# Optimization experiments

Hardware: AMD Instinct MI355X
Metric: run time of the kernel (lower is better)

## Reference

```python
import jax, jax.numpy as jnp
import numpy as np

TOP_K = 3
TEMP = 5.0
EPS = 1e-12

def _normalize(x):
    # F.normalize(dim=-1): x / max(||x||_2, eps)
    n = jnp.linalg.norm(x, axis=-1, keepdims=True)
    return x / jnp.maximum(n, EPS)

def setup_inputs() -> dict:
    key = jax.random.key(0)
    ks = jax.random.split(key, 6)
    B, D, P = 32768, 512, 4096
    return {
        "regime_vector": jax.random.normal(ks[0], (B, D), dtype=jnp.float32),
        "prototypes": jax.random.normal(ks[1], (P, D), dtype=jnp.float32) * 0.1,
        "W1": jax.random.normal(ks[2], (32, 2 * D), dtype=jnp.float32) * 0.02,
        "b1": jax.random.normal(ks[3], (32,), dtype=jnp.float32) * 0.01,
        "W2": jax.random.normal(ks[4], (16, 32), dtype=jnp.float32) * 0.1,
        "b2": jax.random.normal(ks[5], (16,), dtype=jnp.float32) * 0.01,
    }

def reference(regime_vector, prototypes, W1, b1, W2, b2):
    # Cosine similarities: [B, P]
    sims = _normalize(regime_vector) @ _normalize(prototypes).T
    top_sims, top_idx = jax.lax.top_k(sims, TOP_K)          # [B, K]
    weights = jax.nn.softmax(top_sims * TEMP, axis=-1)       # [B, K]
    # Gather candidate prototypes: [B, K, D]
    cand = prototypes[top_idx]
    # Concat(regime, pattern) along feature dim: [B, K, 2D]
    B, K, D = cand.shape
    combined = jnp.concatenate(
        [jnp.broadcast_to(regime_vector[:, None, :], (B, K, D)), cand], axis=-1)
    # Two-layer MLP (torch Linear: x @ W.T + b)
    h = jax.nn.relu(jnp.einsum('bkd,hd->bkh', combined, W1) + b1)  # [B, K, 32]
    feats = jnp.einsum('bkh,oh->bko', h, W2) + b2                  # [B, K, 16]
    # Softmax-weighted sum over the K candidates
    pattern_features = jnp.einsum('bk,bko->bo', weights, feats)    # [B, 16]
    return pattern_features
```

## Files before the change

### kernel.cpp

```cpp
#include <hip/hip_runtime.h>
#include <stdint.h>


#define BDIM 512
#define NB   32768
#define NP   4096

typedef float  f32x4 __attribute__((ext_vector_type(4)));
typedef short  s16x8 __attribute__((ext_vector_type(8)));
typedef unsigned short u16;

__device__ __forceinline__ u16 f2bf(float f) {
  uint32_t u = __float_as_uint(f);
  return (u16)((u + 0x7FFFu + ((u >> 16) & 1u)) >> 16);
}
__device__ __forceinline__ uint32_t mapbf(uint32_t h) {
  return h ^ ((h & 0x8000u) ? 0xFFFFu : 0x8000u);
}
__device__ __forceinline__ uint32_t umx(uint32_t a, uint32_t b) { return a > b ? a : b; }
__device__ __forceinline__ uint32_t umn(uint32_t a, uint32_t b) { return a > b ? b : a; }

__device__ __forceinline__ void ins8(uint32_t* t, uint32_t k) {
#pragma unroll
  for (int i = 0; i < 8; ++i) {
    uint32_t mx = umx(t[i], k), mn = umn(t[i], k);
    t[i] = mx; k = mn;
  }
}

__device__ __forceinline__ void bmerge(uint32_t* a, const uint32_t* b) {
  uint32_t t[8];
#pragma unroll
  for (int i = 0; i < 8; ++i) t[i] = umx(a[i], b[7 - i]);
#pragma unroll
  for (int i = 0; i < 4; ++i) { uint32_t x = umx(t[i], t[i + 4]), y = umn(t[i], t[i + 4]); t[i] = x; t[i + 4] = y; }
#pragma unroll
  for (int g = 0; g < 8; g += 4)
#pragma unroll
    for (int i = 0; i < 2; ++i) { uint32_t x = umx(t[g + i], t[g + i + 2]), y = umn(t[g + i], t[g + i + 2]); t[g + i] = x; t[g + i + 2] = y; }
#pragma unroll
  for (int p = 0; p < 8; p += 2) { uint32_t x = umx(t[p], t[p + 1]), y = umn(t[p], t[p + 1]); t[p] = x; t[p + 1] = y; }
#pragma unroll
  for (int i = 0; i < 8; ++i) a[i] = t[i];
}

__device__ __forceinline__ void mergeshfl(uint32_t* a, int mask) {
  uint32_t b[8];
#pragma unroll
  for (int i = 0; i < 8; ++i) b[i] = (uint32_t)__shfl_xor((int)a[i], mask, 64);
  bmerge(a, b);
}

__global__ __launch_bounds__(256) void prep_kernel(
    const float* __restrict__ src, const float* __restrict__ W1, int w1_off,
    u16* __restrict__ obf, float* __restrict__ onrm, float* __restrict__ oproj,
    float* __restrict__ onf32 )
{
  __shared__ float rows[16][512];
  __shared__ float scratch[8][32];
  const int t = threadIdx.x, l = t & 63, w = t >> 6;
  const long rowbase = (long)blockIdx.x * 16;

  {
    const int r = t >> 4, c0 = (t & 15) * 32;
    const float4* gp = (const float4*)(src + (rowbase + r) * BDIM + c0);
    float4* dp = (float4*)&rows[r][c0];
#pragma unroll
    for (int i = 0; i < 8; ++i) dp[i] = gp[i];
  }
  float wreg[64];
  {
    const int h = t & 31, seg = t >> 5;
    const float* wp = W1 + h * 1024 + w1_off + seg * 64;
#pragma unroll
    for (int i = 0; i < 64; ++i) wreg[i] = wp[i];
  }
  __syncthreads();

#pragma unroll
  for (int i = 0; i < 4; ++i) {
    const int r = w * 4 + i;
    float4 a = *(const float4*)&rows[r][4 * l];
    float4 c = *(const float4*)&rows[r][256 + 4 * l];
    float ss = a.x * a.x + a.y * a.y + a.z * a.z + a.w * a.w
             + c.x * c.x + c.y * c.y + c.z * c.z + c.w * c.w;
#pragma unroll
    for (int msk = 1; msk < 64; msk <<= 1) ss += __shfl_xor(ss, msk, 64);
    const float n = fmaxf(sqrtf(ss), 1e-12f);
    if (l == 0) onrm[rowbase + r] = n;
    float4 qa, qc;
    qa.x = a.x / n; qa.y = a.y / n; qa.z = a.z / n; qa.w = a.w / n;
    qc.x = c.x / n; qc.y = c.y / n; qc.z = c.z / n; qc.w = c.w / n;
    ushort4 u0, u1;
    u0.x = f2bf(qa.x); u0.y = f2bf(qa.y); u0.z = f2bf(qa.z); u0.w = f2bf(qa.w);
    u1.x = f2bf(qc.x); u1.y = f2bf(qc.y); u1.z = f2bf(qc.z); u1.w = f2bf(qc.w);
    *(ushort4*)(obf + (rowbase + r) * BDIM + 4 * l) = u0;
    *(ushort4*)(obf + (rowbase + r) * BDIM + 256 + 4 * l) = u1;
    if (onf32) {
      *(float4*)(onf32 + (rowbase + r) * BDIM + 4 * l) = qa;
      *(float4*)(onf32 + (rowbase + r) * BDIM + 256 + 4 * l) = qc;
    }
  }

  const int h = t & 31, seg = t >> 5;
  for (int r = 0; r < 16; ++r) {
    float p = 0.f;
#pragma unroll
    for (int i = 0; i < 16; ++i) {
      const float4 rv = *(const float4*)&rows[r][seg * 64 + 4 * i];
      p = fmaf(wreg[4 * i + 0], rv.x, p);
      p = fmaf(wreg[4 * i + 1], rv.y, p);
      p = fmaf(wreg[4 * i + 2], rv.z, p);
      p = fmaf(wreg[4 * i + 3], rv.w, p);
    }
    scratch[seg][h] = p;
    __syncthreads();
    if (t < 32) {
      float s2 = 0.f;
#pragma unroll
      for (int sg = 0; sg < 8; ++sg) s2 += scratch[sg][t];
      oproj[(rowbase + r) * 32 + t] = s2;
    }
    __syncthreads();
  }
}

__global__ __launch_bounds__(512, 2) void topk_kernel(
    const u16* __restrict__ An,
    const u16* __restrict__ Bn,
    int* __restrict__ top8out)
{
  __shared__ uint4 smem[3648];
  uint4* As = smem;
  uint4* Bs = smem + 512;
  u16*   dmp = (u16*)(smem + 2560);
  uint32_t* mb = (uint32_t*)smem;

  const int t = threadIdx.x;
  const int l = t & 63;
  const int wid = t >> 6;
  const int wm = wid >> 2;
  const int wn = wid & 3;
  const int g = l >> 4;
  const int m = l & 15;
  const long rb = (long)blockIdx.x * 128;

  const int ar = t >> 2, ac = t & 3;
  const uint4* Agp = (const uint4*)An + (rb + ar) * 64 + ac;
  const uint4* Bgp = (const uint4*)Bn;

  int aIdx[4], bIdx[8];
#pragma unroll
  for (int fm = 0; fm < 4; ++fm) aIdx[fm] = g * 128 + wm * 64 + fm * 16 + m;
#pragma unroll
  for (int fn = 0; fn < 8; ++fn) bIdx[fn] = g * 512 + wn * 128 + fn * 16 + m;

  uint32_t t8[4][8];
#pragma unroll
  for (int a = 0; a < 4; ++a)
#pragma unroll
    for (int i = 0; i < 8; ++i) t8[a][i] = 0u;

  uint4 pa = Agp[0];
  uint4 pb0 = Bgp[(0 + ar) * 64 + ac];
  uint4 pb1 = Bgp[(128 + ar) * 64 + ac];
  uint4 pb2 = Bgp[(256 + ar) * 64 + ac];
  uint4 pb3 = Bgp[(384 + ar) * 64 + ac];

  for (int ni = 0; ni < 8; ++ni) {
    const int n0 = ni * 512;
    f32x4 acc[4][8];
#pragma unroll
    for (int fm = 0; fm < 4; ++fm)
#pragma unroll
      for (int fn = 0; fn < 8; ++fn) acc[fm][fn] = (f32x4){0.f, 0.f, 0.f, 0.f};

    for (int kt = 0; kt < 16; ++kt) {
      __syncthreads();
      As[ac * 128 + ar] = pa;
      Bs[ac * 512 + ar] = pb0;
      Bs[ac * 512 + 128 + ar] = pb1;
      Bs[ac * 512 + 256 + ar] = pb2;
      Bs[ac * 512 + 384 + ar] = pb3;
      {
        int nkt = kt + 1, nni = ni;
        if (nkt == 16) { nkt = 0; ++nni; if (nni == 8) nni = 0; }
        pa = Agp[nkt * 4];
        const long bb = ((long)nni * 512 + ar) * 64 + nkt * 4 + ac;
        pb0 = Bgp[bb];
        pb1 = Bgp[bb + 128 * 64];
        pb2 = Bgp[bb + 256 * 64];
        pb3 = Bgp[bb + 384 * 64];
      }
      __syncthreads();
      uint4 a4[4];
#pragma unroll
      for (int fm = 0; fm < 4; ++fm) a4[fm] = As[aIdx[fm]];
#pragma unroll
      for (int h = 0; h < 2; ++h) {
        uint4 b4[4];
#pragma unroll
        for (int i = 0; i < 4; ++i) b4[i] = Bs[bIdx[4 * h + i]];
#pragma unroll
        for (int fm = 0; fm < 4; ++fm)
#pragma unroll
          for (int i = 0; i < 4; ++i)
            acc[fm][4 * h + i] = __builtin_amdgcn_mfma_f32_16x16x32_bf16(
                __builtin_bit_cast(s16x8, a4[fm]),
                __builtin_bit_cast(s16x8, b4[i]),
                acc[fm][4 * h + i], 0, 0, 0);
      }
    }

#pragma unroll
    for (int fm = 0; fm < 4; ++fm) {
#pragma unroll
      for (int h = 0; h < 2; ++h) {
#pragma unroll
        for (int fi = 0; fi < 4; ++fi)
#pragma unroll
          for (int r = 0; r < 4; ++r)
            dmp[(wid * 16 + 4 * g + r) * 68 + 16 * fi + m] = f2bf(acc[fm][4 * h + fi][r]);
        asm volatile("s_waitcnt lgkmcnt(0)" ::: "memory");
        const int colb = n0 + wn * 128 + h * 64 + g * 16;
#pragma unroll
        for (int j = 0; j < 4; ++j) {
          const uint2 v = *(const uint2*)(dmp + (wid * 16 + m) * 68 + g * 16 + 4 * j);
          const uint32_t k0 = (mapbf(v.x & 0xFFFFu) << 16) | (uint32_t)(colb + 4 * j + 0);
          const uint32_t k1 = (mapbf(v.x >> 16)     << 16) | (uint32_t)(colb + 4 * j + 1);
          const uint32_t k2 = (mapbf(v.y & 0xFFFFu) << 16) | (uint32_t)(colb + 4 * j + 2);
          const uint32_t k3 = (mapbf(v.y >> 16)     << 16) | (uint32_t)(colb + 4 * j + 3);
          const uint32_t mx = umx(umx(k0, k1), umx(k2, k3));
          if (mx > t8[fm][7]) {
            ins8(t8[fm], k0); ins8(t8[fm], k1); ins8(t8[fm], k2); ins8(t8[fm], k3);
          }
        }
      }
    }
  }

  __syncthreads();
#pragma unroll
  for (int fm = 0; fm < 4; ++fm) {
    uint32_t cur[8];
#pragma unroll
    for (int i = 0; i < 8; ++i) cur[i] = t8[fm][i];
    mergeshfl(cur, 16);
    mergeshfl(cur, 32);
    if (l < 16) {
      const int row = wm * 64 + fm * 16 + m;
      uint32_t* dst = mb + row * 36 + wn * 8;
      uint4 u0; u0.x = cur[0]; u0.y = cur[1]; u0.z = cur[2]; u0.w = cur[3];
      uint4 u1; u1.x = cur[4]; u1.y = cur[5]; u1.z = cur[6]; u1.w = cur[7];
      *(uint4*)(dst) = u0;
      *(uint4*)(dst + 4) = u1;
    }
  }
  __syncthreads();
  if (t < 128) {
    const int row = t;
    const uint32_t* src = mb + row * 36;
    uint32_t A8[8], B8[8], C8[8], D8[8];
#pragma unroll
    for (int i = 0; i < 8; ++i) { A8[i] = src[i]; B8[i] = src[8 + i]; C8[i] = src[16 + i]; D8[i] = src[24 + i]; }
    bmerge(A8, B8); bmerge(C8, D8); bmerge(A8, C8);
    int* outp = top8out + (rb + row) * 8;
#pragma unroll
    for (int i = 0; i < 8; ++i) outp[i] = (int)(A8[i] & 0xFFFu);
  }
}

__global__ __launch_bounds__(256) void finalize_kernel(
    const float* __restrict__ regime, const float* __restrict__ protoNf,
    const int* __restrict__ top8, const float* __restrict__ nrm_r,
    const float* __restrict__ rproj, const float* __restrict__ cproj,
    const float* __restrict__ b1, const float* __restrict__ W2,
    const float* __restrict__ b2, float* __restrict__ out)
{
  __shared__ float rlds[4][512];
  const int t = threadIdx.x, l = t & 63, w = t >> 6;
  const long b = (long)blockIdx.x * 4 + w;

  {
    const float n = nrm_r[b];
    const float4* gp = (const float4*)(regime + b * BDIM);
    float4 v0 = gp[l], v1 = gp[64 + l];
    v0.x /= n; v0.y /= n; v0.z /= n; v0.w /= n;
    v1.x /= n; v1.y /= n; v1.z /= n; v1.w /= n;
    *(float4*)&rlds[w][4 * l] = v0;
    *(float4*)&rlds[w][256 + 4 * l] = v1;
  }
  __syncthreads();

  const int j = l >> 3;
  const int pj = top8[b * 8 + j];
  double dd = 0.0;
  {
    const float4* pp = (const float4*)(protoNf + (long)pj * BDIM);
    const float4* rr = (const float4*)&rlds[w][0];
#pragma unroll
    for (int u = 0; u < 16; ++u) {
      const float4 p4 = pp[(l & 7) + 8 * u];
      const float4 r4 = rr[(l & 7) + 8 * u];
      dd = fma((double)p4.x, (double)r4.x, dd);
      dd = fma((double)p4.y, (double)r4.y, dd);
      dd = fma((double)p4.z, (double)r4.z, dd);
      dd = fma((double)p4.w, (double)r4.w, dd);
    }
  }
  dd += __shfl_xor(dd, 1, 64);
  dd += __shfl_xor(dd, 2, 64);
  dd += __shfl_xor(dd, 4, 64);

  double sall[8]; int pall[8];
#pragma unroll
  for (int q = 0; q < 8; ++q) {
    sall[q] = __shfl(dd, q * 8, 64);
    pall[q] = __shfl(pj, q * 8, 64);
  }
  double vv[3]; int ppi[3]; unsigned chosen = 0;
#pragma unroll
  for (int r = 0; r < 3; ++r) {
    double bv = -1e300; int bp = 0x7FFFFFFF; int bq = 0;
#pragma unroll
    for (int q = 0; q < 8; ++q) {
      const bool ex = (chosen >> q) & 1u;
      const bool better = !ex && ((sall[q] > bv) || (sall[q] == bv && pall[q] < bp));
      bv = better ? sall[q] : bv;
      bp = better ? pall[q] : bp;
      bq = better ? q : bq;
    }
    vv[r] = bv; ppi[r] = bp; chosen |= 1u << bq;
  }
  const float v0f = (float)vv[0], v1f = (float)vv[1], v2f = (float)vv[2];
  const float e1 = expf(5.f * (v1f - v0f));
  const float e2 = expf(5.f * (v2f - v0f));
  const float winv = 1.f / (1.f + e1 + e2);
  const float w0 = winv, w1 = e1 * winv, w2 = e2 * winv;

  const int hu = l & 31, o = l & 15;
  const float rpv = rproj[b * 32 + hu];
  const float b1v = b1[hu];
  float w2row[32];
#pragma unroll
  for (int hh = 0; hh < 32; ++hh) w2row[hh] = W2[o * 32 + hh];
  float outacc = (l < 16) ? b2[o] : 0.f;
#pragma unroll
  for (int k = 0; k < 3; ++k) {
    const float cpv = cproj[(long)ppi[k] * 32 + hu];
    const float hval = fmaxf(rpv + cpv + b1v, 0.f);
    float f = 0.f;
#pragma unroll
    for (int hh = 0; hh < 32; ++hh) f = fmaf(w2row[hh], __shfl(hval, hh, 64), f);
    const float wk = (k == 0) ? w0 : ((k == 1) ? w1 : w2);
    outacc = fmaf(wk, f, outacc);
  }
  if (l < 16) out[b * 16 + o] = outacc;
}

extern "C" void kernel_launch(void* const* d_in, const int* in_sizes, int n_in,
                              void* d_out, int out_size, void* d_ws, size_t ws_size,
                              hipStream_t stream)
{
  (void)in_sizes; (void)n_in; (void)out_size; (void)ws_size;
  const float* regime = (const float*)d_in[0];
  const float* protos = (const float*)d_in[1];
  const float* W1     = (const float*)d_in[2];
  const float* b1     = (const float*)d_in[3];
  const float* W2     = (const float*)d_in[4];
  const float* b2     = (const float*)d_in[5];
  float* out = (float*)d_out;

  char* ws = (char*)d_ws;
  u16*   protoN  = (u16*)ws;    ws += (size_t)NP * BDIM * 2;
  u16*   regimeN = (u16*)ws;    ws += (size_t)NB * BDIM * 2;
  float* nrm_p   = (float*)ws;  ws += (size_t)NP * 4;
  float* nrm_r   = (float*)ws;  ws += (size_t)NB * 4;
  float* cproj   = (float*)ws;  ws += (size_t)NP * 32 * 4;
  float* rproj   = (float*)ws;  ws += (size_t)NB * 32 * 4;
  int*   top8    = (int*)ws;    ws += (size_t)NB * 8 * 4;
  float* protoNf = (float*)ws;

  hipLaunchKernelGGL(prep_kernel, dim3(NP / 16), dim3(256), 0, stream,
                     protos, W1, 512, protoN, nrm_p, cproj, protoNf);
  hipLaunchKernelGGL(prep_kernel, dim3(NB / 16), dim3(256), 0, stream,
                     regime, W1, 0, regimeN, nrm_r, rproj, (float*)nullptr);
  hipLaunchKernelGGL(topk_kernel, dim3(NB / 128), dim3(512), 0, stream,
                     regimeN, protoN, top8);
  hipLaunchKernelGGL(finalize_kernel, dim3(NB / 4), dim3(256), 0, stream,
                     regime, protoNf, top8, nrm_r, rproj, cproj, b1, W2, b2, out);
}
```

Before: 480.4 us.

## Rewrite top-k GEMM with direct global-to-LDS double buffering and fp32 top-3 keys

```diff
diff --git a/kernel.cpp b/kernel.cpp
--- a/kernel.cpp
+++ b/kernel.cpp
@@ -5,27 +5,35 @@
 #define BDIM 512
 #define NB   32768
 #define NP   4096
+#define PCH  256
 
 typedef float  f32x4 __attribute__((ext_vector_type(4)));
 typedef short  s16x8 __attribute__((ext_vector_type(8)));
 typedef unsigned short u16;
 
+typedef const __attribute__((address_space(1))) unsigned int* gas_t;
+typedef __attribute__((address_space(3))) unsigned int* las_t;
+
+__device__ __forceinline__ void gll16(const void* g, void* l) {
+  __builtin_amdgcn_global_load_lds((gas_t)g, (las_t)l, 16, 0, 0);
+}
+
 __device__ __forceinline__ u16 f2bf(float f) {
   uint32_t u = __float_as_uint(f);
   return (u16)((u + 0x7FFFu + ((u >> 16) & 1u)) >> 16);
 }
-__device__ __forceinline__ uint32_t mapbf(uint32_t h) {
-  return h ^ ((h & 0x8000u) ? 0xFFFFu : 0x8000u);
-}
 __device__ __forceinline__ uint32_t umx(uint32_t a, uint32_t b) { return a > b ? a : b; }
 __device__ __forceinline__ uint32_t umn(uint32_t a, uint32_t b) { return a > b ? b : a; }
 
-__device__ __forceinline__ void ins8(uint32_t* t, uint32_t k) {
-#pragma unroll
-  for (int i = 0; i < 8; ++i) {
-    uint32_t mx = umx(t[i], k), mn = umn(t[i], k);
-    t[i] = mx; k = mn;
-  }
+__device__ __forceinline__ uint32_t packkey(float v, int col) {
+  uint32_t u = __float_as_uint(v);
+  uint32_t mp = u ^ (uint32_t)(((int)u >> 31) | 0x80000000);
+  return (mp & 0xFFFFF000u) | (uint32_t)col;
+}
+__device__ __forceinline__ float unpackf(uint32_t k) {
+  uint32_t mbits = k & 0xFFFFF000u;
+  uint32_t u = (mbits & 0x80000000u) ? (mbits ^ 0x80000000u) : ~mbits;
+  return __uint_as_float(u);
 }
 
 __device__ __forceinline__ void bmerge(uint32_t* a, const uint32_t* b) {
@@ -43,7 +51,6 @@
 #pragma unroll
   for (int i = 0; i < 8; ++i) a[i] = t[i];
 }
-
 __device__ __forceinline__ void mergeshfl(uint32_t* a, int mask) {
   uint32_t b[8];
 #pragma unroll
@@ -53,11 +60,11 @@
 
 __global__ __launch_bounds__(256) void prep_kernel(
     const float* __restrict__ src, const float* __restrict__ W1, int w1_off,
-    u16* __restrict__ obf, float* __restrict__ onrm, float* __restrict__ oproj,
-    float* __restrict__ onf32 )
+    int mode, u16* __restrict__ obf, float* __restrict__ onrm,
+    float* __restrict__ oproj, float* __restrict__ onf32)
 {
   __shared__ float rows[16][512];
-  __shared__ float scratch[8][32];
+  __shared__ float pscr[16][8][32];
   const int t = threadIdx.x, l = t & 63, w = t >> 6;
   const long rowbase = (long)blockIdx.x * 16;
 
@@ -80,6 +87,7 @@
 #pragma unroll
   for (int i = 0; i < 4; ++i) {
     const int r = w * 4 + i;
+    const long row = rowbase + r;
     float4 a = *(const float4*)&rows[r][4 * l];
     float4 c = *(const float4*)&rows[r][256 + 4 * l];
     float ss = a.x * a.x + a.y * a.y + a.z * a.z + a.w * a.w
@@ -87,18 +95,22 @@
 #pragma unroll
     for (int msk = 1; msk < 64; msk <<= 1) ss += __shfl_xor(ss, msk, 64);
     const float n = fmaxf(sqrtf(ss), 1e-12f);
-    if (l == 0) onrm[rowbase + r] = n;
     float4 qa, qc;
     qa.x = a.x / n; qa.y = a.y / n; qa.z = a.z / n; qa.w = a.w / n;
     qc.x = c.x / n; qc.y = c.y / n; qc.z = c.z / n; qc.w = c.w / n;
     ushort4 u0, u1;
     u0.x = f2bf(qa.x); u0.y = f2bf(qa.y); u0.z = f2bf(qa.z); u0.w = f2bf(qa.w);
     u1.x = f2bf(qc.x); u1.y = f2bf(qc.y); u1.z = f2bf(qc.z); u1.w = f2bf(qc.w);
-    *(ushort4*)(obf + (rowbase + r) * BDIM + 4 * l) = u0;
-    *(ushort4*)(obf + (rowbase + r) * BDIM + 256 + 4 * l) = u1;
-    if (onf32) {
-      *(float4*)(onf32 + (rowbase + r) * BDIM + 4 * l) = qa;
-      *(float4*)(onf32 + (rowbase + r) * BDIM + 256 + 4 * l) = qc;
+    if (mode == 0) {
+      if (l == 0) onrm[row] = n;
+      *(ushort4*)(obf + row * BDIM + 4 * l) = u0;
+      *(ushort4*)(obf + row * BDIM + 256 + 4 * l) = u1;
+    } else {
+      char* base = (char*)obf;
+      *(ushort4*)(base + ((long)(l >> 4) * NP + row) * 128 + 8 * (l & 15)) = u0;
+      *(ushort4*)(base + ((long)(4 + (l >> 4)) * NP + row) * 128 + 8 * (l & 15)) = u1;
+      *(float4*)(onf32 + row * BDIM + 4 * l) = qa;
+      *(float4*)(onf32 + row * BDIM + 256 + 4 * l) = qc;
     }
   }
 
@@ -106,173 +118,172 @@
   for (int r = 0; r < 16; ++r) {
     float p = 0.f;
 #pragma unroll
-    for (int i = 0; i < 16; ++i) {
-      const float4 rv = *(const float4*)&rows[r][seg * 64 + 4 * i];
-      p = fmaf(wreg[4 * i + 0], rv.x, p);
-      p = fmaf(wreg[4 * i + 1], rv.y, p);
-      p = fmaf(wreg[4 * i + 2], rv.z, p);
-      p = fmaf(wreg[4 * i + 3], rv.w, p);
-    }
-    scratch[seg][h] = p;
-    __syncthreads();
-    if (t < 32) {
-      float s2 = 0.f;
-#pragma unroll
-      for (int sg = 0; sg < 8; ++sg) s2 += scratch[sg][t];
-      oproj[(rowbase + r) * 32 + t] = s2;
-    }
-    __syncthreads();
-  }
-}
-
-__global__ __launch_bounds__(512, 2) void topk_kernel(
-    const u16* __restrict__ An,
-    const u16* __restrict__ Bn,
-    int* __restrict__ top8out)
+    for (int j = 0; j < 16; ++j) {
+      const float4 rv = *(const float4*)&rows[r][seg * 64 + 4 * j];
+      p = fmaf(wreg[4 * j + 0], rv.x, p);
+      p = fmaf(wreg[4 * j + 1], rv.y, p);
+      p = fmaf(wreg[4 * j + 2], rv.z, p);
+      p = fmaf(wreg[4 * j + 3], rv.w, p);
+    }
+    pscr[r][seg][h] = p;
+  }
+  __syncthreads();
+#pragma unroll
+  for (int q = 0; q < 2; ++q) {
+    const int idx = t + q * 256;
+    const int rr = idx >> 5, hh = idx & 31;
+    float s = 0.f;
+#pragma unroll
+    for (int sg = 0; sg < 8; ++sg) s += pscr[rr][sg][hh];
+    oproj[(rowbase + rr) * 32 + hh] = s;
+  }
+}
+
+__global__ __launch_bounds__(256, 2) void topk_kernel(
+    const u16* __restrict__ Rn,
+    const u16* __restrict__ Pk,
+    uint32_t* __restrict__ keys8)
 {
-  __shared__ uint4 smem[3648];
-  uint4* As = smem;
-  uint4* Bs = smem + 512;
-  u16*   dmp = (u16*)(smem + 2560);
-  uint32_t* mb = (uint32_t*)smem;
-
-  const int t = threadIdx.x;
-  const int l = t & 63;
-  const int wid = t >> 6;
-  const int wm = wid >> 2;
-  const int wn = wid & 3;
-  const int g = l >> 4;
-  const int m = l & 15;
-  const long rb = (long)blockIdx.x * 128;
-
-  const int ar = t >> 2, ac = t & 3;
-  const uint4* Agp = (const uint4*)An + (rb + ar) * 64 + ac;
-  const uint4* Bgp = (const uint4*)Bn;
-
-  int aIdx[4], bIdx[8];
-#pragma unroll
-  for (int fm = 0; fm < 4; ++fm) aIdx[fm] = g * 128 + wm * 64 + fm * 16 + m;
-#pragma unroll
-  for (int fn = 0; fn < 8; ++fn) bIdx[fn] = g * 512 + wn * 128 + fn * 16 + m;
-
-  uint32_t t8[4][8];
-#pragma unroll
-  for (int a = 0; a < 4; ++a)
-#pragma unroll
-    for (int i = 0; i < 8; ++i) t8[a][i] = 0u;
-
-  uint4 pa = Agp[0];
-  uint4 pb0 = Bgp[(0 + ar) * 64 + ac];
-  uint4 pb1 = Bgp[(128 + ar) * 64 + ac];
-  uint4 pb2 = Bgp[(256 + ar) * 64 + ac];
-  uint4 pb3 = Bgp[(384 + ar) * 64 + ac];
-
-  for (int ni = 0; ni < 8; ++ni) {
-    const int n0 = ni * 512;
-    f32x4 acc[4][8];
-#pragma unroll
-    for (int fm = 0; fm < 4; ++fm)
-#pragma unroll
-      for (int fn = 0; fn < 8; ++fn) acc[fm][fn] = (f32x4){0.f, 0.f, 0.f, 0.f};
-
-    for (int kt = 0; kt < 16; ++kt) {
-      __syncthreads();
-      As[ac * 128 + ar] = pa;
-      Bs[ac * 512 + ar] = pb0;
-      Bs[ac * 512 + 128 + ar] = pb1;
-      Bs[ac * 512 + 256 + ar] = pb2;
-      Bs[ac * 512 + 384 + ar] = pb3;
-      {
-        int nkt = kt + 1, nni = ni;
-        if (nkt == 16) { nkt = 0; ++nni; if (nni == 8) nni = 0; }
-        pa = Agp[nkt * 4];
-        const long bb = ((long)nni * 512 + ar) * 64 + nkt * 4 + ac;
-        pb0 = Bgp[bb];
-        pb1 = Bgp[bb + 128 * 64];
-        pb2 = Bgp[bb + 256 * 64];
-        pb3 = Bgp[bb + 384 * 64];
-      }
-      __syncthreads();
-      uint4 a4[4];
-#pragma unroll
-      for (int fm = 0; fm < 4; ++fm) a4[fm] = As[aIdx[fm]];
-#pragma unroll
-      for (int h = 0; h < 2; ++h) {
-        uint4 b4[4];
-#pragma unroll
-        for (int i = 0; i < 4; ++i) b4[i] = Bs[bIdx[4 * h + i]];
-#pragma unroll
-        for (int fm = 0; fm < 4; ++fm)
-#pragma unroll
-          for (int i = 0; i < 4; ++i)
-            acc[fm][4 * h + i] = __builtin_amdgcn_mfma_f32_16x16x32_bf16(
-                __builtin_bit_cast(s16x8, a4[fm]),
-                __builtin_bit_cast(s16x8, b4[i]),
-                acc[fm][4 * h + i], 0, 0, 0);
-      }
-    }
-
-#pragma unroll
-    for (int fm = 0; fm < 4; ++fm) {
-#pragma unroll
-      for (int h = 0; h < 2; ++h) {
-#pragma unroll
-        for (int fi = 0; fi < 4; ++fi)
-#pragma unroll
-          for (int r = 0; r < 4; ++r)
-            dmp[(wid * 16 + 4 * g + r) * 68 + 16 * fi + m] = f2bf(acc[fm][4 * h + fi][r]);
-        asm volatile("s_waitcnt lgkmcnt(0)" ::: "memory");
-        const int colb = n0 + wn * 128 + h * 64 + g * 16;
-#pragma unroll
-        for (int j = 0; j < 4; ++j) {
-          const uint2 v = *(const uint2*)(dmp + (wid * 16 + m) * 68 + g * 16 + 4 * j);
-          const uint32_t k0 = (mapbf(v.x & 0xFFFFu) << 16) | (uint32_t)(colb + 4 * j + 0);
-          const uint32_t k1 = (mapbf(v.x >> 16)     << 16) | (uint32_t)(colb + 4 * j + 1);
-          const uint32_t k2 = (mapbf(v.y & 0xFFFFu) << 16) | (uint32_t)(colb + 4 * j + 2);
-          const uint32_t k3 = (mapbf(v.y >> 16)     << 16) | (uint32_t)(colb + 4 * j + 3);
-          const uint32_t mx = umx(umx(k0, k1), umx(k2, k3));
-          if (mx > t8[fm][7]) {
-            ins8(t8[fm], k0); ins8(t8[fm], k1); ins8(t8[fm], k2); ins8(t8[fm], k3);
-          }
+  __shared__ uint4 lds4[5120];
+  char* ldsb = (char*)lds4;
+
+  const int t = threadIdx.x, l = t & 63, wid = t >> 6;
+  const int wp = wid >> 1;
+  const int wr = wid & 1;
+  const int g = l >> 4, m = l & 15;
+  const long rb = (long)blockIdx.x * 64;
+  const char* Pkb = (const char*)Pk;
+  const char* Rnb = (const char*)Rn;
+  const int swsrc = 16 * ((l & 7) ^ ((l >> 3) & 7));
+  const int lrow8 = (l >> 3);
+
+  f32x4 acc[8][2];
+  uint32_t k3[2][3];
+  float thr[2];
+#pragma unroll
+  for (int fn = 0; fn < 2; ++fn) {
+    thr[fn] = -1e30f;
+#pragma unroll
+    for (int i = 0; i < 3; ++i) k3[fn][i] = 0u;
+  }
+
+#define ISSUE(buf, ni_, kp_)                                                   \
+  do {                                                                         \
+    char* lp_ = ldsb + (buf) * 40960;                                          \
+    const char* pg = Pkb + ((long)(kp_) * NP + (ni_) * PCH) * 128;             \
+    _Pragma("unroll")                                                          \
+    for (int i_ = 0; i_ < 8; ++i_) {                                           \
+      const int ch_ = wid * 8 + i_;                                            \
+      gll16(pg + ch_ * 1024 + lrow8 * 128 + swsrc, lp_ + ch_ * 1024);          \
+    }                                                                          \
+    _Pragma("unroll")                                                          \
+    for (int j_ = 0; j_ < 2; ++j_) {                                           \
+      const int ch_ = wid * 2 + j_;                                            \
+      gll16(Rnb + (rb + ch_ * 8 + lrow8) * 1024 + (kp_) * 128 + swsrc,         \
+            lp_ + 32768 + ch_ * 1024);                                         \
+    }                                                                          \
+  } while (0)
+
+  ISSUE(0, 0, 0);
+
+  for (int ni = 0; ni < 16; ++ni) {
+#pragma unroll
+    for (int fm = 0; fm < 8; ++fm)
+#pragma unroll
+      for (int fn = 0; fn < 2; ++fn) acc[fm][fn] = (f32x4){0.f, 0.f, 0.f, 0.f};
+
+    for (int kp = 0; kp < 8; ++kp) {
+      const int ph = ni * 8 + kp;
+      asm volatile("s_waitcnt vmcnt(0)" ::: "memory");
+      __builtin_amdgcn_s_barrier();
+      const int nph = ph + 1;
+      if (nph < 128) ISSUE(nph & 1, nph >> 3, nph & 7);
+      __builtin_amdgcn_sched_barrier(0);
+      const char* lp = ldsb + (ph & 1) * 40960;
+      const char* lr = lp + 32768;
+      const int sw = 16 * (m & 7);
+#pragma unroll
+      for (int ks = 0; ks < 2; ++ks) {
+        const int koff = (ks * 64 + 16 * g) ^ sw;
+        const char* pbr = lr + (wr * 32 + m) * 128 + koff;
+        const char* pa = lp + (wp * 128 + m) * 128 + koff;
+        uint4 b0 = *(const uint4*)(pbr);
+        uint4 b1 = *(const uint4*)(pbr + 2048);
+#pragma unroll
+        for (int fm = 0; fm < 8; ++fm) {
+          uint4 a4 = *(const uint4*)(pa + fm * 2048);
+          acc[fm][0] = __builtin_amdgcn_mfma_f32_16x16x32_bf16(
+              __builtin_bit_cast(s16x8, a4), __builtin_bit_cast(s16x8, b0),
+              acc[fm][0], 0, 0, 0);
+          acc[fm][1] = __builtin_amdgcn_mfma_f32_16x16x32_bf16(
+              __builtin_bit_cast(s16x8, a4), __builtin_bit_cast(s16x8, b1),
+              acc[fm][1], 0, 0, 0);
         }
       }
     }
-  }
-
+
+    const int pb0 = ni * PCH + wp * 128 + 4 * g;
+#pragma unroll
+    for (int fn = 0; fn < 2; ++fn) {
+#pragma unroll
+      for (int fm = 0; fm < 8; ++fm) {
+        const f32x4 v = acc[fm][fn];
+        const float m4 = fmaxf(fmaxf(v[0], v[1]), fmaxf(v[2], v[3]));
+        if (m4 > thr[fn]) {
+#pragma unroll
+          for (int r = 0; r < 4; ++r) {
+            uint32_t kk = packkey(v[r], pb0 + fm * 16 + r);
+            uint32_t mx0 = umx(k3[fn][0], kk), mn0 = umn(k3[fn][0], kk);
+            k3[fn][0] = mx0; kk = mn0;
+            uint32_t mx1 = umx(k3[fn][1], kk), mn1 = umn(k3[fn][1], kk);
+            k3[fn][1] = mx1; kk = mn1;
+            k3[fn][2] = umx(k3[fn][2], kk);
+          }
+          thr[fn] = unpackf(k3[fn][2]);
+        }
+      }
+    }
+  }
+#undef ISSUE
+
+  uint32_t* mrg = (uint32_t*)ldsb;
+  uint32_t cur[2][8];
+#pragma unroll
+  for (int fn = 0; fn < 2; ++fn) {
+    cur[fn][0] = k3[fn][0]; cur[fn][1] = k3[fn][1]; cur[fn][2] = k3[fn][2];
+#pragma unroll
+    for (int i = 3; i < 8; ++i) cur[fn][i] = 0u;
+    mergeshfl(cur[fn], 16);
+    mergeshfl(cur[fn], 32);
+  }
   __syncthreads();
 #pragma unroll
-  for (int fm = 0; fm < 4; ++fm) {
-    uint32_t cur[8];
-#pragma unroll
-    for (int i = 0; i < 8; ++i) cur[i] = t8[fm][i];
-    mergeshfl(cur, 16);
-    mergeshfl(cur, 32);
-    if (l < 16) {
-      const int row = wm * 64 + fm * 16 + m;
-      uint32_t* dst = mb + row * 36 + wn * 8;
-      uint4 u0; u0.x = cur[0]; u0.y = cur[1]; u0.z = cur[2]; u0.w = cur[3];
-      uint4 u1; u1.x = cur[4]; u1.y = cur[5]; u1.z = cur[6]; u1.w = cur[7];
-      *(uint4*)(dst) = u0;
-      *(uint4*)(dst + 4) = u1;
-    }
-  }
+  for (int fn = 0; fn < 2; ++fn)
+    if (wp == 1 && g == fn) {
+      uint32_t* d = mrg + (wr * 32 + fn * 16 + m) * 8;
+      uint4 a; a.x = cur[fn][0]; a.y = cur[fn][1]; a.z = cur[fn][2]; a.w = cur[fn][3];
+      uint4 b; b.x = cur[fn][4]; b.y = cur[fn][5]; b.z = cur[fn][6]; b.w = cur[fn][7];
+      *(uint4*)(d) = a; *(uint4*)(d + 4) = b;
+    }
   __syncthreads();
-  if (t < 128) {
-    const int row = t;
-    const uint32_t* src = mb + row * 36;
-    uint32_t A8[8], B8[8], C8[8], D8[8];
-#pragma unroll
-    for (int i = 0; i < 8; ++i) { A8[i] = src[i]; B8[i] = src[8 + i]; C8[i] = src[16 + i]; D8[i] = src[24 + i]; }
-    bmerge(A8, B8); bmerge(C8, D8); bmerge(A8, C8);
-    int* outp = top8out + (rb + row) * 8;
-#pragma unroll
-    for (int i = 0; i < 8; ++i) outp[i] = (int)(A8[i] & 0xFFFu);
-  }
+#pragma unroll
+  for (int fn = 0; fn < 2; ++fn)
+    if (wp == 0 && g == fn) {
+      const int row = wr * 32 + fn * 16 + m;
+      uint32_t oth[8];
+#pragma unroll
+      for (int i = 0; i < 8; ++i) oth[i] = mrg[row * 8 + i];
+      bmerge(cur[fn], oth);
+      uint32_t* d = keys8 + (rb + row) * 8;
+      uint4 a; a.x = cur[fn][0]; a.y = cur[fn][1]; a.z = cur[fn][2]; a.w = cur[fn][3];
+      uint4 b; b.x = cur[fn][4]; b.y = cur[fn][5]; b.z = cur[fn][6]; b.w = cur[fn][7];
+      *(uint4*)(d) = a; *(uint4*)(d + 4) = b;
+    }
 }
 
 __global__ __launch_bounds__(256) void finalize_kernel(
     const float* __restrict__ regime, const float* __restrict__ protoNf,
-    const int* __restrict__ top8, const float* __restrict__ nrm_r,
+    const uint32_t* __restrict__ keys8, const float* __restrict__ nrm_r,
     const float* __restrict__ rproj, const float* __restrict__ cproj,
     const float* __restrict__ b1, const float* __restrict__ W2,
     const float* __restrict__ b2, float* __restrict__ out)
@@ -293,7 +304,9 @@
   __syncthreads();
 
   const int j = l >> 3;
-  const int pj = top8[b * 8 + j];
+  const uint32_t key = keys8[b * 8 + j];
+  const int pj = (int)(key & 0xFFFu);
+
   double dd = 0.0;
   {
     const float4* pp = (const float4*)(protoNf + (long)pj * BDIM);
@@ -321,7 +334,7 @@
   double vv[3]; int ppi[3]; unsigned chosen = 0;
 #pragma unroll
   for (int r = 0; r < 3; ++r) {
-    double bv = -1e300; int bp = 0x7FFFFFFF; int bq = 0;
+    double bv = -1e301; int bp = 0x7FFFFFFF; int bq = 0;
 #pragma unroll
     for (int q = 0; q < 8; ++q) {
       const bool ex = (chosen >> q) & 1u;
@@ -372,21 +385,20 @@
   float* out = (float*)d_out;
 
   char* ws = (char*)d_ws;
-  u16*   protoN  = (u16*)ws;    ws += (size_t)NP * BDIM * 2;
-  u16*   regimeN = (u16*)ws;    ws += (size_t)NB * BDIM * 2;
-  float* nrm_p   = (float*)ws;  ws += (size_t)NP * 4;
-  float* nrm_r   = (float*)ws;  ws += (size_t)NB * 4;
-  float* cproj   = (float*)ws;  ws += (size_t)NP * 32 * 4;
-  float* rproj   = (float*)ws;  ws += (size_t)NB * 32 * 4;
-  int*   top8    = (int*)ws;    ws += (size_t)NB * 8 * 4;
-  float* protoNf = (float*)ws;
+  u16*      protoK  = (u16*)ws;      ws += (size_t)NP * BDIM * 2;
+  u16*      regimeN = (u16*)ws;      ws += (size_t)NB * BDIM * 2;
+  float*    protoNf = (float*)ws;    ws += (size_t)NP * BDIM * 4;
+  float*    nrm_r   = (float*)ws;    ws += (size_t)NB * 4;
+  float*    cproj   = (float*)ws;    ws += (size_t)NP * 32 * 4;
+  float*    rproj   = (float*)ws;    ws += (size_t)NB * 32 * 4;
+  uint32_t* keys8   = (uint32_t*)ws; ws += (size_t)NB * 8 * 4;
 
   hipLaunchKernelGGL(prep_kernel, dim3(NP / 16), dim3(256), 0, stream,
-                     protos, W1, 512, protoN, nrm_p, cproj, protoNf);
+                     protos, W1, 512, 1, protoK, (float*)nullptr, cproj, protoNf);
   hipLaunchKernelGGL(prep_kernel, dim3(NB / 16), dim3(256), 0, stream,
-                     regime, W1, 0, regimeN, nrm_r, rproj, (float*)nullptr);
-  hipLaunchKernelGGL(topk_kernel, dim3(NB / 128), dim3(512), 0, stream,
-                     regimeN, protoN, top8);
+                     regime, W1, 0, 0, regimeN, nrm_r, rproj, (float*)nullptr);
+  hipLaunchKernelGGL(topk_kernel, dim3(512), dim3(256), 0, stream,
+                     regimeN, protoK, keys8);
   hipLaunchKernelGGL(finalize_kernel, dim3(NB / 4), dim3(256), 0, stream,
-                     regime, protoNf, top8, nrm_r, rproj, cproj, b1, W2, b2, out);
-}
+                     regime, protoNf, keys8, nrm_r, rproj, cproj, b1, W2, b2, out);
+}
```

Result: faster. 425.6 us (-11.4%).
